# Kernel optimization log

Measured on AMD Instinct MI355X. Metric: run time of the kernel, lower is better.

Reference implementation:

```python
import jax, jax.numpy as jnp
import numpy as np

# pool sizes (must match init_kwargs)
N_FQK, N_FV, N_REL, N_VAL, N_KNOW = 512, 256, 128, 32, 256
K_FQK, K_FV, K_REL, K_VAL = 64, 32, 16, 3
D_MODEL, D_SPACE = 1024, 64
B, S = 8, 2048


def _topk_sparsify(w, k):
    # keep top-k entries per row, zero the rest (values unchanged)
    vals, idx = jax.lax.top_k(w, k)                      # [B,k]
    out = jnp.zeros_like(w)
    rows = jnp.arange(w.shape[0])[:, None]
    return out.at[rows, idx].set(vals), idx


def setup_inputs() -> dict:
    key = jax.random.key(0)
    k1, k2, k3, k4 = jax.random.split(key, 4)
    x = jax.random.normal(k1, (B, S, D_MODEL), dtype=jnp.float32)
    # importance: per-token weights normalized over sequence
    importance = jax.nn.softmax(jax.random.normal(k2, (B, S), dtype=jnp.float32), axis=-1)
    W = jax.random.normal(k3, (D_MODEL, D_SPACE), dtype=jnp.float32) * 0.02
    b = jnp.zeros((D_SPACE,), dtype=jnp.float32)
    total = N_FQK + N_FV + N_REL + N_VAL + N_KNOW
    neuron_emb = jax.random.normal(k4, (total, D_SPACE), dtype=jnp.float32) * 0.02
    return {"x": x, "importance": importance, "W": W, "b": b, "neuron_emb": neuron_emb}


def reference(x, importance, W, b, neuron_emb):
    # projection (dropout inactive in eval); normalized neuron embeddings
    h = x @ W + b                                         # [B,S,d_space]
    emb_n = neuron_emb / jnp.linalg.norm(neuron_emb, axis=-1, keepdims=True)
    all_logits = jnp.einsum('bsd,nd->bsn', h, emb_n)      # [B,S,N_total]

    e0 = N_FQK
    e1 = e0 + N_FV
    e2 = e1 + N_REL
    e3 = e2 + N_VAL

    def route(lo, hi):
        pref = jax.nn.softmax(all_logits[..., lo:hi], axis=-1)  # [B,S,n]
        w = jnp.einsum('bs,bsn->bn', importance, pref)          # [B,n]
        return pref, w

    _, w_qk = route(0, e0)
    _, idx_qk = jax.lax.top_k(w_qk, K_FQK)
    idx_qk = jnp.sort(idx_qk, axis=-1)

    _, w_v = route(e0, e1)
    _, idx_v = jax.lax.top_k(w_v, K_FV)
    idx_v = jnp.sort(idx_v, axis=-1)

    # relational Q and K share the same logit slice (eval: no excitability bonus)
    _, w_rQ = route(e1, e2)
    _, w_rK = route(e1, e2)
    rw_Q, _ = _topk_sparsify(w_rQ, K_REL)
    rw_K, _ = _topk_sparsify(w_rK, K_REL)

    _, w_val = route(e2, e3)
    vw, _ = _topk_sparsify(w_val, K_VAL)

    return idx_qk, idx_v, rw_Q, rw_K, vw, w_qk, w_v
```

## Files before the change

### kernel.cpp

```cpp
#include <hip/hip_runtime.h>
#include <hip/hip_bf16.h>
#include <hip/hip_fp16.h>
#include <math.h>

#define ROWS  16384
#define DM    1024
#define DS    64
#define NUSE  928
#define NPAD  960
#define RPB   32
#define NBLK  (ROWS/RPB)

typedef __attribute__((ext_vector_type(8))) short bf16x8;
typedef __attribute__((ext_vector_type(4))) float f32x4;

static __device__ inline f32x4 mfma16(bf16x8 a, bf16x8 b, f32x4 c) {
    return __builtin_amdgcn_mfma_f32_16x16x32_bf16(a, b, c, 0, 0, 0);
}

static __device__ inline void bfsplit(float v, unsigned short& h, unsigned short& l) {
    unsigned u = __float_as_uint(v);
    unsigned hr = u + 0x7FFFu + ((u >> 16) & 1u);
    h = (unsigned short)(hr >> 16);
    float hf = __uint_as_float((unsigned)h << 16);
    float r = v - hf;
    unsigned ur = __float_as_uint(r);
    unsigned lr2 = ur + 0x7FFFu + ((ur >> 16) & 1u);
    l = (unsigned short)(lr2 >> 16);
}

#define OFF_EBH  0LL
#define OFF_EBL  122880LL
#define OFF_WBH  245760LL
#define OFF_WBL  376832LL
#define OFF_WP   507904LL
#define OFF_WR   2473984LL

__global__ __launch_bounds__(256) void k_prep(const float* __restrict__ emb,
                                              const float* __restrict__ W,
                                              unsigned short* __restrict__ ebh,
                                              unsigned short* __restrict__ ebl,
                                              unsigned short* __restrict__ wbh,
                                              unsigned short* __restrict__ wbl) {
    if (blockIdx.x < 4) {
        int n = blockIdx.x * 256 + threadIdx.x;
        if (n >= NPAD) return;
        if (n >= NUSE) {
            #pragma unroll
            for (int d = 0; d < DS; d++) {
                int kt = d >> 5, q = (d >> 3) & 3, j = d & 7;
                int a = ((kt * 4 + q) * NPAD + n) * 8 + j;
                ebh[a] = 0; ebl[a] = 0;
            }
            return;
        }
        float ss = 0.f;
        #pragma unroll
        for (int d = 0; d < DS; d++) { float v = emb[n * DS + d]; ss = fmaf(v, v, ss); }
        float inv = 1.0f / sqrtf(ss);
        #pragma unroll
        for (int d = 0; d < DS; d++) {
            float v = emb[n * DS + d] * inv;
            unsigned short h, l; bfsplit(v, h, l);
            int kt = d >> 5, q = (d >> 3) & 3, j = d & 7;
            int a = ((kt * 4 + q) * NPAD + n) * 8 + j;
            ebh[a] = h; ebl[a] = l;
        }
    } else {
        int idx = (blockIdx.x - 4) * 256 + threadIdx.x;
        int ktg = idx >> 6, n = idx & 63;
        #pragma unroll
        for (int q = 0; q < 4; q++) {
            #pragma unroll
            for (int j = 0; j < 8; j++) {
                int k = ktg * 32 + q * 8 + j;
                float v = W[k * DS + n];
                unsigned short h, l; bfsplit(v, h, l);
                int a = ((ktg * 4 + q) * 64 + n) * 8 + j;
                wbh[a] = h; wbl[a] = l;
            }
        }
    }
}

__global__ __launch_bounds__(512, 4) void k_mega(const float* __restrict__ x,
                                                 const float* __restrict__ bias,
                                                 const unsigned short* __restrict__ wbh,
                                                 const unsigned short* __restrict__ wbl,
                                                 const unsigned short* __restrict__ ebh,
                                                 const unsigned short* __restrict__ ebl,
                                                 const float* __restrict__ imp,
                                                 float* __restrict__ wpart) {
    __shared__ __align__(16) unsigned char smem[79872];
    unsigned short* Ph    = (unsigned short*)smem;
    float*          Cb    = (float*)smem;
    unsigned short* Hh    = (unsigned short*)(smem + 69120);
    unsigned short* Hl    = (unsigned short*)(smem + 73216);
    float*          zslot = (float*)(smem + 77312);
    float*          coefL = (float*)(smem + 79360);

    const int tid = threadIdx.x;
    const int rc = blockIdx.x;
    const long long row0 = (long long)rc * RPB;
    const int w = tid >> 6, lane = tid & 63, q = lane >> 4, lm = lane & 15;

    zslot[tid] = 0.f;

    const int rg = w >> 2, kg = w & 3;
    const int srow = tid >> 4, sjg = tid & 15;
    const int skt = sjg >> 2, sq = sjg & 3;
    const int sidx = ((skt * 4 + sq) * 32 + srow) * 8;
    const float* xp = &x[(row0 + srow) * (long long)DM + sjg * 8];

    f32x4 acc[4];
    #pragma unroll
    for (int f = 0; f < 4; f++) { acc[f].x = 0.f; acc[f].y = 0.f; acc[f].z = 0.f; acc[f].w = 0.f; }

    float4 pv0 = *(const float4*)&xp[0];
    float4 pv1 = *(const float4*)&xp[4];
    {
        union { uint4 u; unsigned short s[8]; } ah, al;
        bfsplit(pv0.x, ah.s[0], al.s[0]); bfsplit(pv0.y, ah.s[1], al.s[1]);
        bfsplit(pv0.z, ah.s[2], al.s[2]); bfsplit(pv0.w, ah.s[3], al.s[3]);
        bfsplit(pv1.x, ah.s[4], al.s[4]); bfsplit(pv1.y, ah.s[5], al.s[5]);
        bfsplit(pv1.z, ah.s[6], al.s[6]); bfsplit(pv1.w, ah.s[7], al.s[7]);
        *(uint4*)&((unsigned short*)(smem))[sidx]         = ah.u;
        *(uint4*)&((unsigned short*)(smem + 16384))[sidx] = al.u;
    }

    for (int ch = 0; ch < 8; ch++) {
        if (ch < 7) {
            pv0 = *(const float4*)&xp[(ch + 1) * 128];
            pv1 = *(const float4*)&xp[(ch + 1) * 128 + 4];
        }
        __syncthreads();
        {
            const unsigned short* XhB = (const unsigned short*)(smem + (ch & 1) * 8192);
            const unsigned short* XlB = (const unsigned short*)(smem + 16384 + (ch & 1) * 8192);
            const bf16x8 a_h = *(const bf16x8*)&XhB[((kg * 4 + q) * 32 + rg * 16 + lm) * 8];
            const bf16x8 a_l = *(const bf16x8*)&XlB[((kg * 4 + q) * 32 + rg * 16 + lm) * 8];
            const int ktg = ch * 4 + kg;
            #pragma unroll
            for (int f = 0; f < 4; f++) {
                const int ba = ((ktg * 4 + q) * 64 + f * 16 + lm) * 8;
                const bf16x8 b_h = *(const bf16x8*)&wbh[ba];
                const bf16x8 b_l = *(const bf16x8*)&wbl[ba];
                acc[f] = mfma16(a_h, b_h, acc[f]);
                acc[f] = mfma16(a_h, b_l, acc[f]);
                acc[f] = mfma16(a_l, b_h, acc[f]);
            }
        }
        if (ch < 7) {
            union { uint4 u; unsigned short s[8]; } ah, al;
            bfsplit(pv0.x, ah.s[0], al.s[0]); bfsplit(pv0.y, ah.s[1], al.s[1]);
            bfsplit(pv0.z, ah.s[2], al.s[2]); bfsplit(pv0.w, ah.s[3], al.s[3]);
            bfsplit(pv1.x, ah.s[4], al.s[4]); bfsplit(pv1.y, ah.s[5], al.s[5]);
            bfsplit(pv1.z, ah.s[6], al.s[6]); bfsplit(pv1.w, ah.s[7], al.s[7]);
            *(uint4*)&((unsigned short*)(smem + ((ch + 1) & 1) * 8192))[sidx]         = ah.u;
            *(uint4*)&((unsigned short*)(smem + 16384 + ((ch + 1) & 1) * 8192))[sidx] = al.u;
        }
    }
    __syncthreads();

    #pragma unroll
    for (int f = 0; f < 4; f++)
        #pragma unroll
        for (int t = 0; t < 4; t++)
            Cb[w * 1088 + (q * 4 + t) * 68 + f * 16 + lm] = acc[f][t];
    __syncthreads();

    {
        const int r = tid >> 4, seg = tid & 15;
        const int rgg = r >> 4, rl = r & 15;
        const int c0 = seg * 4;
        float4 s = *(const float4*)&bias[c0];
        #pragma unroll
        for (int g = 0; g < 4; g++) {
            float4 a = *(const float4*)&Cb[(rgg * 4 + g) * 1088 + rl * 68 + c0];
            s.x += a.x; s.y += a.y; s.z += a.z; s.w += a.w;
        }
        __syncthreads();
        unsigned short h0, l0, h1, l1, h2, l2, h3, l3;
        bfsplit(s.x, h0, l0); bfsplit(s.y, h1, l1);
        bfsplit(s.z, h2, l2); bfsplit(s.w, h3, l3);
        const int ktH = c0 >> 5, qH = (c0 >> 3) & 3, jH = c0 & 7;
        const int base = ((ktH * 4 + qH) * 32 + r) * 8 + jH;
        uint2 ph; ph.x = (unsigned)h0 | ((unsigned)h1 << 16); ph.y = (unsigned)h2 | ((unsigned)h3 << 16);
        uint2 pl; pl.x = (unsigned)l0 | ((unsigned)l1 << 16); pl.y = (unsigned)l2 | ((unsigned)l3 << 16);
        *(uint2*)&Hh[base] = ph;
        *(uint2*)&Hl[base] = pl;
    }
    __syncthreads();

    const int wg = w & 3, rgp = w >> 2;
    bf16x8 a_h[2], a_l[2];
    #pragma unroll
    for (int kt = 0; kt < 2; kt++) {
        const int ab = ((kt * 4 + q) * 32 + rgp * 16 + lm) * 8;
        a_h[kt] = *(const bf16x8*)&Hh[ab];
        a_l[kt] = *(const bf16x8*)&Hl[ab];
    }

    #pragma unroll
    for (int v = 0; v < 4; v++) {
        const int nt = wg + v * 4;
        if (nt > 14) continue;
        f32x4 acc2[4];
        #pragma unroll
        for (int f = 0; f < 4; f++) { acc2[f].x = 0.f; acc2[f].y = 0.f; acc2[f].z = 0.f; acc2[f].w = 0.f; }
        #pragma unroll
        for (int kt = 0; kt < 2; kt++) {
            #pragma unroll
            for (int f = 0; f < 4; f++) {
                const int bb = ((kt * 4 + q) * NPAD + nt * 64 + f * 16 + lm) * 8;
                const bf16x8 b_h = *(const bf16x8*)&ebh[bb];
                const bf16x8 b_l = *(const bf16x8*)&ebl[bb];
                acc2[f] = mfma16(a_h[kt], b_h, acc2[f]);
                acc2[f] = mfma16(a_h[kt], b_l, acc2[f]);
                acc2[f] = mfma16(a_l[kt], b_h, acc2[f]);
            }
        }
        const int sl = (nt < 8) ? 0 : (nt < 12) ? 1 : (nt < 14) ? 2 : 3;
        float s0 = 0.f, s1 = 0.f, s2 = 0.f, s3 = 0.f;
        #pragma unroll
        for (int f = 0; f < 4; f++) {
            float e0 = __expf(acc2[f][0]);
            float e1 = __expf(acc2[f][1]);
            float e2 = __expf(acc2[f][2]);
            float e3 = __expf(acc2[f][3]);
            const int n = nt * 64 + f * 16 + lm;
            unsigned short p0 = __half_as_ushort(__float2half(e0));
            unsigned short p1 = __half_as_ushort(__float2half(e1));
            unsigned short p2 = __half_as_ushort(__float2half(e2));
            unsigned short p3 = __half_as_ushort(__float2half(e3));
            uint2 pk; pk.x = (unsigned)p0 | ((unsigned)p1 << 16); pk.y = (unsigned)p2 | ((unsigned)p3 << 16);
            *(uint2*)&Ph[n * 36 + rgp * 16 + q * 4] = pk;
            if (nt * 64 + f * 16 < NUSE) {
                s0 += e0; s1 += e1; s2 += e2; s3 += e3;
            }
        }
        #pragma unroll
        for (int off = 1; off < 16; off <<= 1) {
            s0 += __shfl_xor(s0, off); s1 += __shfl_xor(s1, off);
            s2 += __shfl_xor(s2, off); s3 += __shfl_xor(s3, off);
        }
        if (lm < 4) {
            float sv = (lm == 0) ? s0 : (lm == 1) ? s1 : (lm == 2) ? s2 : s3;
            zslot[(wg * 4 + sl) * 32 + rgp * 16 + q * 4 + lm] += sv;
        }
    }
    __syncthreads();

    if (tid < 32) {
        const int r = tid;
        const float im = imp[row0 + r];
        #pragma unroll
        for (int sl = 0; sl < 4; sl++) {
            float Z = zslot[(0 * 4 + sl) * 32 + r] + zslot[(1 * 4 + sl) * 32 + r]
                    + zslot[(2 * 4 + sl) * 32 + r] + zslot[(3 * 4 + sl) * 32 + r];
            coefL[r * 4 + sl] = im / Z;
        }
    }
    __syncthreads();

    for (int nn = tid; nn < NUSE; nn += 512) {
        const int sl = (nn < 512) ? 0 : (nn < 768) ? 1 : (nn < 896) ? 2 : 3;
        float accw = 0.f;
        #pragma unroll
        for (int rb = 0; rb < 8; rb++) {
            uint2 pk = *(const uint2*)&Ph[nn * 36 + rb * 4];
            float v0 = __half2float(__ushort_as_half((unsigned short)(pk.x & 0xFFFF)));
            float v1 = __half2float(__ushort_as_half((unsigned short)(pk.x >> 16)));
            float v2 = __half2float(__ushort_as_half((unsigned short)(pk.y & 0xFFFF)));
            float v3 = __half2float(__ushort_as_half((unsigned short)(pk.y >> 16)));
            const int row = rb * 4;
            accw = fmaf(coefL[(row + 0) * 4 + sl], v0, accw);
            accw = fmaf(coefL[(row + 1) * 4 + sl], v1, accw);
            accw = fmaf(coefL[(row + 2) * 4 + sl], v2, accw);
            accw = fmaf(coefL[(row + 3) * 4 + sl], v3, accw);
        }
        wpart[(long long)rc * NPAD + nn] = accw;
    }
}

__global__ __launch_bounds__(256) void k_red(const float* __restrict__ wpart,
                                             float* __restrict__ wred) {
    const int g = blockIdx.x;
    const int b = blockIdx.y;
    const int tid = threadIdx.x;
    const int n = g * 32 + (tid & 31);
    const int cp = tid >> 5;
    float s = 0.f;
    #pragma unroll 2
    for (int c = cp; c < 64; c += 8)
        s += wpart[(long long)(b * 64 + c) * NPAD + n];
    __shared__ float red[8][32];
    red[cp][tid & 31] = s;
    __syncthreads();
    if (tid < 32) {
        float t = 0.f;
        #pragma unroll
        for (int p = 0; p < 8; p++) t += red[p][tid];
        wred[b * 960 + g * 32 + tid] = t;
    }
}

__global__ __launch_bounds__(512) void k_rank(const float* __restrict__ wred,
                                              float* __restrict__ out) {
    const int b = blockIdx.x;
    const int tid = threadIdx.x;
    __shared__ float w_s[NUSE];
    __shared__ int   rk[NUSE];

    for (int n = tid; n < NUSE; n += 512) {
        float s = wred[b * 960 + n];
        w_s[n] = s;
        if (n < 512)      out[3072 + (long long)b * 512 + n] = s;
        else if (n < 768) out[7168 + (long long)b * 256 + (n - 512)] = s;
    }
    __syncthreads();

    for (int n = tid; n < NUSE; n += 512) {
        int lo, hi;
        if (n < 512)      { lo = 0;   hi = 512; }
        else if (n < 768) { lo = 512; hi = 768; }
        else if (n < 896) { lo = 768; hi = 896; }
        else              { lo = 896; hi = NUSE; }
        float wn = w_s[n];
        int r = 0;
        for (int m = lo; m < hi; m++) {
            float wm = w_s[m];
            r += (wm > wn) || ((wm == wn) && (m < n));
        }
        rk[n] = r;
    }
    __syncthreads();

    if (tid < 512) {
        int n = tid;
        if (rk[n] < 64) {
            int pos = 0;
            for (int m = 0; m < n; m++) pos += (rk[m] < 64) ? 1 : 0;
            out[(long long)b * 64 + pos] = (float)n;
        }
    }
    if (tid < 256) {
        int n = 512 + tid;
        if (rk[n] < 32) {
            int pos = 0;
            for (int m = 512; m < n; m++) pos += (rk[m] < 32) ? 1 : 0;
            out[512 + (long long)b * 32 + pos] = (float)tid;
        }
    }
    if (tid < 128) {
        int n = 768 + tid;
        float v = (rk[n] < 16) ? w_s[n] : 0.f;
        out[768 + (long long)b * 128 + tid] = v;
        out[1792 + (long long)b * 128 + tid] = v;
    }
    if (tid < 32) {
        int n = 896 + tid;
        float v = (rk[n] < 3) ? w_s[n] : 0.f;
        out[2816 + (long long)b * 32 + tid] = v;
    }
}

extern "C" void kernel_launch(void* const* d_in, const int* in_sizes, int n_in,
                              void* d_out, int out_size, void* d_ws, size_t ws_size,
                              hipStream_t stream) {
    const float* x    = (const float*)d_in[0];
    const float* imp  = (const float*)d_in[1];
    const float* W    = (const float*)d_in[2];
    const float* bias = (const float*)d_in[3];
    const float* emb  = (const float*)d_in[4];

    char* ws = (char*)d_ws;
    unsigned short* ebh = (unsigned short*)(ws + OFF_EBH);
    unsigned short* ebl = (unsigned short*)(ws + OFF_EBL);
    unsigned short* wbh = (unsigned short*)(ws + OFF_WBH);
    unsigned short* wbl = (unsigned short*)(ws + OFF_WBL);
    float* wpart        = (float*)(ws + OFF_WP);
    float* wred         = (float*)(ws + OFF_WR);
    float* out          = (float*)d_out;

    k_prep<<<12, 256, 0, stream>>>(emb, W, ebh, ebl, wbh, wbl);
    k_mega<<<NBLK, 512, 0, stream>>>(x, bias, wbh, wbl, ebh, ebl, imp, wpart);
    k_red<<<dim3(29, 8), 256, 0, stream>>>(wpart, wred);
    k_rank<<<8, 512, 0, stream>>>(wred, out);
}
```

Measured before the change: 158.6 us.

## Swizzle x tile in LDS and double-buffer weight/embedding register prefetch

Replaces the LDS layout of the bf16-split x tile with an XOR-swizzled layout to reduce bank conflicts on the fragment reads. It also prefetches the next chunk of W fragments, and likewise the next embedding fragments in the logit GEMM, into double-buffered registers so global loads overlap the MFMAs. The logit loop is flattened into 8 steps with clamped tile indices and a liveness guard. The cost is higher register pressure, which may reduce occupancy.

```diff
diff --git a/kernel.cpp b/kernel.cpp
--- a/kernel.cpp
+++ b/kernel.cpp
@@ -108,8 +108,8 @@
 
     const int rg = w >> 2, kg = w & 3;
     const int srow = tid >> 4, sjg = tid & 15;
-    const int skt = sjg >> 2, sq = sjg & 3;
-    const int sidx = ((skt * 4 + sq) * 32 + srow) * 8;
+    const int sunit = srow * 16 + (sjg ^ (srow & 15));
+    const int runit = (rg * 16 + lm) * 16 + ((kg * 4 + q) ^ lm);
     const float* xp = &x[(row0 + srow) * (long long)DM + sjg * 8];
 
     f32x4 acc[4];
@@ -124,31 +124,43 @@
         bfsplit(pv0.z, ah.s[2], al.s[2]); bfsplit(pv0.w, ah.s[3], al.s[3]);
         bfsplit(pv1.x, ah.s[4], al.s[4]); bfsplit(pv1.y, ah.s[5], al.s[5]);
         bfsplit(pv1.z, ah.s[6], al.s[6]); bfsplit(pv1.w, ah.s[7], al.s[7]);
-        *(uint4*)&((unsigned short*)(smem))[sidx]         = ah.u;
-        *(uint4*)&((unsigned short*)(smem + 16384))[sidx] = al.u;
-    }
-
+        *(uint4*)&((unsigned short*)(smem))[sunit * 8]         = ah.u;
+        *(uint4*)&((unsigned short*)(smem + 16384))[sunit * 8] = al.u;
+    }
+    bf16x8 Wh[2][4], Wl[2][4];
+    #pragma unroll
+    for (int f = 0; f < 4; f++) {
+        const int ba = ((kg * 4 + q) * 64 + f * 16 + lm) * 8;
+        Wh[0][f] = *(const bf16x8*)&wbh[ba];
+        Wl[0][f] = *(const bf16x8*)&wbl[ba];
+    }
+
+    #pragma unroll
     for (int ch = 0; ch < 8; ch++) {
+        const int p = ch & 1;
         if (ch < 7) {
             pv0 = *(const float4*)&xp[(ch + 1) * 128];
             pv1 = *(const float4*)&xp[(ch + 1) * 128 + 4];
         }
         __syncthreads();
-        {
-            const unsigned short* XhB = (const unsigned short*)(smem + (ch & 1) * 8192);
-            const unsigned short* XlB = (const unsigned short*)(smem + 16384 + (ch & 1) * 8192);
-            const bf16x8 a_h = *(const bf16x8*)&XhB[((kg * 4 + q) * 32 + rg * 16 + lm) * 8];
-            const bf16x8 a_l = *(const bf16x8*)&XlB[((kg * 4 + q) * 32 + rg * 16 + lm) * 8];
-            const int ktg = ch * 4 + kg;
+        const unsigned short* XhB = (const unsigned short*)(smem + p * 8192);
+        const unsigned short* XlB = (const unsigned short*)(smem + 16384 + p * 8192);
+        const bf16x8 a_h = *(const bf16x8*)&XhB[runit * 8];
+        const bf16x8 a_l = *(const bf16x8*)&XlB[runit * 8];
+        if (ch < 7) {
+            const int ktg = (ch + 1) * 4 + kg;
             #pragma unroll
             for (int f = 0; f < 4; f++) {
                 const int ba = ((ktg * 4 + q) * 64 + f * 16 + lm) * 8;
-                const bf16x8 b_h = *(const bf16x8*)&wbh[ba];
-                const bf16x8 b_l = *(const bf16x8*)&wbl[ba];
-                acc[f] = mfma16(a_h, b_h, acc[f]);
-                acc[f] = mfma16(a_h, b_l, acc[f]);
-                acc[f] = mfma16(a_l, b_h, acc[f]);
-            }
+                Wh[p ^ 1][f] = *(const bf16x8*)&wbh[ba];
+                Wl[p ^ 1][f] = *(const bf16x8*)&wbl[ba];
+            }
+        }
+        #pragma unroll
+        for (int f = 0; f < 4; f++) {
+            acc[f] = mfma16(a_h, Wh[p][f], acc[f]);
+            acc[f] = mfma16(a_h, Wl[p][f], acc[f]);
+            acc[f] = mfma16(a_l, Wh[p][f], acc[f]);
         }
         if (ch < 7) {
             union { uint4 u; unsigned short s[8]; } ah, al;
@@ -156,8 +168,8 @@
             bfsplit(pv0.z, ah.s[2], al.s[2]); bfsplit(pv0.w, ah.s[3], al.s[3]);
             bfsplit(pv1.x, ah.s[4], al.s[4]); bfsplit(pv1.y, ah.s[5], al.s[5]);
             bfsplit(pv1.z, ah.s[6], al.s[6]); bfsplit(pv1.w, ah.s[7], al.s[7]);
-            *(uint4*)&((unsigned short*)(smem + ((ch + 1) & 1) * 8192))[sidx]         = ah.u;
-            *(uint4*)&((unsigned short*)(smem + 16384 + ((ch + 1) & 1) * 8192))[sidx] = al.u;
+            *(uint4*)&((unsigned short*)(smem + (p ^ 1) * 8192))[sunit * 8]         = ah.u;
+            *(uint4*)&((unsigned short*)(smem + 16384 + (p ^ 1) * 8192))[sunit * 8] = al.u;
         }
     }
     __syncthreads();
@@ -201,52 +213,75 @@
         a_l[kt] = *(const bf16x8*)&Hl[ab];
     }
 
-    #pragma unroll
-    for (int v = 0; v < 4; v++) {
-        const int nt = wg + v * 4;
-        if (nt > 14) continue;
-        f32x4 acc2[4];
-        #pragma unroll
-        for (int f = 0; f < 4; f++) { acc2[f].x = 0.f; acc2[f].y = 0.f; acc2[f].z = 0.f; acc2[f].w = 0.f; }
-        #pragma unroll
-        for (int kt = 0; kt < 2; kt++) {
+    int ntA[4];
+    #pragma unroll
+    for (int v = 0; v < 4; v++) { int nt = wg + v * 4; ntA[v] = (nt > 14) ? 14 : nt; }
+    const bool v3ok = (wg < 3);
+
+    bf16x8 Bh[2][4], Bl[2][4];
+    #pragma unroll
+    for (int f = 0; f < 4; f++) {
+        const int bb = ((0 * 4 + q) * NPAD + ntA[0] * 64 + f * 16 + lm) * 8;
+        Bh[0][f] = *(const bf16x8*)&ebh[bb];
+        Bl[0][f] = *(const bf16x8*)&ebl[bb];
+    }
+
+    f32x4 acc2[4];
+    #pragma unroll
+    for (int s = 0; s < 8; s++) {
+        const int v = s >> 1, kt = s & 1, p = s & 1;
+        if (kt == 0) {
+            #pragma unroll
+            for (int f = 0; f < 4; f++) { acc2[f].x = 0.f; acc2[f].y = 0.f; acc2[f].z = 0.f; acc2[f].w = 0.f; }
+        }
+        if (s < 7) {
+            const int vn = (s + 1) >> 1, ktn = (s + 1) & 1;
             #pragma unroll
             for (int f = 0; f < 4; f++) {
-                const int bb = ((kt * 4 + q) * NPAD + nt * 64 + f * 16 + lm) * 8;
-                const bf16x8 b_h = *(const bf16x8*)&ebh[bb];
-                const bf16x8 b_l = *(const bf16x8*)&ebl[bb];
-                acc2[f] = mfma16(a_h[kt], b_h, acc2[f]);
-                acc2[f] = mfma16(a_h[kt], b_l, acc2[f]);
-                acc2[f] = mfma16(a_l[kt], b_h, acc2[f]);
-            }
-        }
-        const int sl = (nt < 8) ? 0 : (nt < 12) ? 1 : (nt < 14) ? 2 : 3;
-        float s0 = 0.f, s1 = 0.f, s2 = 0.f, s3 = 0.f;
-        #pragma unroll
-        for (int f = 0; f < 4; f++) {
-            float e0 = __expf(acc2[f][0]);
-            float e1 = __expf(acc2[f][1]);
-            float e2 = __expf(acc2[f][2]);
-            float e3 = __expf(acc2[f][3]);
-            const int n = nt * 64 + f * 16 + lm;
-            unsigned short p0 = __half_as_ushort(__float2half(e0));
-            unsigned short p1 = __half_as_ushort(__float2half(e1));
-            unsigned short p2 = __half_as_ushort(__float2half(e2));
-            unsigned short p3 = __half_as_ushort(__float2half(e3));
-            uint2 pk; pk.x = (unsigned)p0 | ((unsigned)p1 << 16); pk.y = (unsigned)p2 | ((unsigned)p3 << 16);
-            *(uint2*)&Ph[n * 36 + rgp * 16 + q * 4] = pk;
-            if (nt * 64 + f * 16 < NUSE) {
-                s0 += e0; s1 += e1; s2 += e2; s3 += e3;
-            }
-        }
-        #pragma unroll
-        for (int off = 1; off < 16; off <<= 1) {
-            s0 += __shfl_xor(s0, off); s1 += __shfl_xor(s1, off);
-            s2 += __shfl_xor(s2, off); s3 += __shfl_xor(s3, off);
-        }
-        if (lm < 4) {
-            float sv = (lm == 0) ? s0 : (lm == 1) ? s1 : (lm == 2) ? s2 : s3;
-            zslot[(wg * 4 + sl) * 32 + rgp * 16 + q * 4 + lm] += sv;
+                const int bb = ((ktn * 4 + q) * NPAD + ntA[vn] * 64 + f * 16 + lm) * 8;
+                Bh[p ^ 1][f] = *(const bf16x8*)&ebh[bb];
+                Bl[p ^ 1][f] = *(const bf16x8*)&ebl[bb];
+            }
+        }
+        const bool live = (v < 3) || v3ok;
+        if (live) {
+            #pragma unroll
+            for (int f = 0; f < 4; f++) {
+                acc2[f] = mfma16(a_h[kt], Bh[p][f], acc2[f]);
+                acc2[f] = mfma16(a_h[kt], Bl[p][f], acc2[f]);
+                acc2[f] = mfma16(a_l[kt], Bh[p][f], acc2[f]);
+            }
+        }
+        if (kt == 1 && live) {
+            const int nt = wg + v * 4;
+            const int sl = (nt < 8) ? 0 : (nt < 12) ? 1 : (nt < 14) ? 2 : 3;
+            float s0 = 0.f, s1 = 0.f, s2 = 0.f, s3 = 0.f;
+            #pragma unroll
+            for (int f = 0; f < 4; f++) {
+                float e0 = __expf(acc2[f][0]);
+                float e1 = __expf(acc2[f][1]);
+                float e2 = __expf(acc2[f][2]);
+                float e3 = __expf(acc2[f][3]);
+                const int n = nt * 64 + f * 16 + lm;
+                unsigned short p0 = __half_as_ushort(__float2half(e0));
+                unsigned short p1 = __half_as_ushort(__float2half(e1));
+                unsigned short p2 = __half_as_ushort(__float2half(e2));
+                unsigned short p3 = __half_as_ushort(__float2half(e3));
+                uint2 pk; pk.x = (unsigned)p0 | ((unsigned)p1 << 16); pk.y = (unsigned)p2 | ((unsigned)p3 << 16);
+                *(uint2*)&Ph[n * 36 + rgp * 16 + q * 4] = pk;
+                if (nt * 64 + f * 16 < NUSE) {
+                    s0 += e0; s1 += e1; s2 += e2; s3 += e3;
+                }
+            }
+            #pragma unroll
+            for (int off = 1; off < 16; off <<= 1) {
+                s0 += __shfl_xor(s0, off); s1 += __shfl_xor(s1, off);
+                s2 += __shfl_xor(s2, off); s3 += __shfl_xor(s3, off);
+            }
+            if (lm < 4) {
+                float sv = (lm == 0) ? s0 : (lm == 1) ? s1 : (lm == 2) ? s2 : s3;
+                zslot[(wg * 4 + sl) * 32 + rgp * 16 + q * 4 + lm] += sv;
+            }
         }
     }
     __syncthreads();
```

Result: no change. 158.6 us (+0.0%).
